# Performance work log

Measured on AMD Instinct MI355X. Metric: run time of the kernel, lower is better.

## Reference

```python
import jax, jax.numpy as jnp
import numpy as np

LN_EPS = 1e-5
N, D = 512, 512


def setup_inputs() -> dict:
    key = jax.random.key(0)
    ks = jax.random.split(key, 3)
    s1 = 1.0 / np.sqrt(2 * D)  # torch Linear default-ish scale
    s2 = 1.0 / np.sqrt(D)
    return {
        "embeddings": jax.random.normal(ks[0], (N, D), jnp.float32),
        "W1": jax.random.normal(ks[1], (2 * D, D), jnp.float32) * s1,  # [in, out]
        "b1": jnp.zeros((D,), jnp.float32),
        "gamma": jnp.ones((D,), jnp.float32),
        "beta": jnp.zeros((D,), jnp.float32),
        "W2": jax.random.normal(ks[2], (D, 1), jnp.float32) * s2,
        "b2": jnp.zeros((1,), jnp.float32),
    }


def reference(embeddings, W1, b1, gamma, beta, W2, b2):
    d = embeddings.shape[-1]
    # Linear(2D -> D) on cat(e_i, e_j) decomposes into two GEMMs + broadcast add,
    # avoiding materializing the [N, N, 2D] concatenated pair tensor.
    left = embeddings @ W1[:d]              # [N, D]  (contribution of e_i)
    right = embeddings @ W1[d:] + b1        # [N, D]  (contribution of e_j + bias)
    h = left[:, None, :] + right[None, :, :]  # [N, N, D]
    # LayerNorm over last dim (eps matches torch default)
    mu = h.mean(axis=-1, keepdims=True)
    var = ((h - mu) ** 2).mean(axis=-1, keepdims=True)
    h = (h - mu) * jax.lax.rsqrt(var + LN_EPS) * gamma + beta
    # exact GELU (torch nn.GELU default)
    h = jax.nn.gelu(h, approximate=False)
    s = jax.nn.sigmoid(jnp.squeeze(h @ W2, -1) + b2[0])  # [N, N]
    # original loop only evaluates pairs i <= j and mirrors to (j, i)
    n = s.shape[0]
    upper = jnp.arange(n)[:, None] <= jnp.arange(n)[None, :]
    return jnp.where(upper, s, s.T)
```

## Files before the change

kernel.cpp:

```cpp
#include <hip/hip_runtime.h>


#define N_ 512
#define D_ 512

__global__ __launch_bounds__(512) void k_gemm(const float* __restrict__ E,
                                              const float* __restrict__ W1,
                                              const float* __restrict__ b1,
                                              float* __restrict__ W ) {
    __shared__ float et[512 * 20];

    const int t = threadIdx.x;
    const int bg = blockIdx.x;
    const int rg = bg >> 4;
    const int cg = bg & 15;
    const int r0 = rg * 16;
    const int half = cg >> 3;
    const int cb = (cg & 7) << 6;

    for (int x = t; x < 16 * 128; x += 512) {
        const int r = x >> 7, k4 = (x & 127) << 2;
        float4 v = *(const float4*)&E[(r0 + r) * D_ + k4];
        et[(k4 + 0) * 20 + r] = v.x;
        et[(k4 + 1) * 20 + r] = v.y;
        et[(k4 + 2) * 20 + r] = v.z;
        et[(k4 + 3) * 20 + r] = v.w;
    }
    __syncthreads();

    const int lane = t & 63;
    const int ks = t >> 6;
    const int kb = ks << 6;
    const int c4 = (lane & 15) << 2;
    const int rq = ((lane >> 4) & 3) << 2;
    const float* __restrict__ wp = W1 + (half << 18) + (kb << 9) + cb + c4;

    float4 a0 = {0.f, 0.f, 0.f, 0.f}, a1 = {0.f, 0.f, 0.f, 0.f};
    float4 a2 = {0.f, 0.f, 0.f, 0.f}, a3 = {0.f, 0.f, 0.f, 0.f};
#pragma unroll 16
    for (int k = 0; k < 64; ++k) {
        float4 wv = *(const float4*)(wp + (k << 9));
        float4 ev = *(const float4*)&et[(kb + k) * 20 + rq];
        a0.x = fmaf(ev.x, wv.x, a0.x); a0.y = fmaf(ev.x, wv.y, a0.y);
        a0.z = fmaf(ev.x, wv.z, a0.z); a0.w = fmaf(ev.x, wv.w, a0.w);
        a1.x = fmaf(ev.y, wv.x, a1.x); a1.y = fmaf(ev.y, wv.y, a1.y);
        a1.z = fmaf(ev.y, wv.z, a1.z); a1.w = fmaf(ev.y, wv.w, a1.w);
        a2.x = fmaf(ev.z, wv.x, a2.x); a2.y = fmaf(ev.z, wv.y, a2.y);
        a2.z = fmaf(ev.z, wv.z, a2.z); a2.w = fmaf(ev.z, wv.w, a2.w);
        a3.x = fmaf(ev.w, wv.x, a3.x); a3.y = fmaf(ev.w, wv.y, a3.y);
        a3.z = fmaf(ev.w, wv.z, a3.z); a3.w = fmaf(ev.w, wv.w, a3.w);
    }

    __syncthreads();
    float* red = et;
    const int ob = (ks << 10) + c4;
    *(float4*)&red[ob + ((rq + 0) << 6)] = a0;
    *(float4*)&red[ob + ((rq + 1) << 6)] = a1;
    *(float4*)&red[ob + ((rq + 2) << 6)] = a2;
    *(float4*)&red[ob + ((rq + 3) << 6)] = a3;
    __syncthreads();

    float2 s = {0.f, 0.f};
#pragma unroll
    for (int k2 = 0; k2 < 8; ++k2) {
        float2 p = *(const float2*)&red[(k2 << 10) + (t << 1)];
        s.x += p.x; s.y += p.y;
    }
    const int ro = t >> 5, co = (t << 1) & 63;
    if (half) {
        float2 bb = *(const float2*)&b1[cb + co];
        s.x += bb.x; s.y += bb.y;
    }
    *(float2*)&W[((half << 9) + r0 + ro) * D_ + cb + co] = s;
}


#define GELU1(L, R, G, BE, WC, RST, T2N, ACC)                                 \
    do {                                                                      \
        float s_ = (L) + (R);                                                 \
        float x_ = fmaf(fmaf(s_, (RST), (T2N)), (G), (BE));                   \
        float q_ = x_ * fmaf(-0.10294340f, x_ * x_, -2.30220935f);            \
        float e_ = __builtin_amdgcn_exp2f(q_);                                \
        float ge_ = x_ * __builtin_amdgcn_rcpf(1.f + e_);                     \
        ACC = fmaf(ge_, (WC), ACC);                                           \
    } while (0)

#define GELU4(LQ, RQ, RST, T2N, ACC)                                          \
    do {                                                                      \
        GELU1(LQ.x, RQ.x, g4.x, be4.x, w4.x, RST, T2N, ACC);                  \
        GELU1(LQ.y, RQ.y, g4.y, be4.y, w4.y, RST, T2N, ACC);                  \
        GELU1(LQ.z, RQ.z, g4.z, be4.z, w4.z, RST, T2N, ACC);                  \
        GELU1(LQ.w, RQ.w, g4.w, be4.w, w4.w, RST, T2N, ACC);                  \
    } while (0)

#define DOT4(LQ, RQ, ACC)                                                     \
    ACC += LQ.x * RQ.x + LQ.y * RQ.y + LQ.z * RQ.z + LQ.w * RQ.w

#define BFLY(V)                                                               \
    do {                                                                      \
        V += __shfl_xor(V, 1, 64);                                            \
        V += __shfl_xor(V, 2, 64);                                            \
        V += __shfl_xor(V, 4, 64);                                            \
        V += __shfl_xor(V, 8, 64);                                            \
    } while (0)

__global__ __launch_bounds__(256, 4) void k_pair(const float* __restrict__ W,
                                                 const float* __restrict__ gf,
                                                 const float* __restrict__ bef,
                                                 const float* __restrict__ wf,
                                                 const float* __restrict__ b2f,
                                                 float* __restrict__ out) {
    __shared__ float ls[8][516];
    __shared__ float rs[8][516];
    __shared__ float smean[16];
    __shared__ float svar[16];

    const int b = blockIdx.x;
    int I = (int)((129.0f - sqrtf(16641.0f - 8.0f * (float)b)) * 0.5f);
    if (I < 0) I = 0;
    if (I > 63) I = 63;
#define S_(i) (64 * (i) - ((i) * ((i)-1)) / 2)
    while (S_(I) > b) --I;
    while (S_(I + 1) <= b) ++I;
    const int J = I + (b - S_(I));
#undef S_

    const int t = threadIdx.x;
    const int ks = t & 15;
    const int pt = t >> 4;
    const int i1 = pt & 7;
    const int j4 = (pt >> 3) * 4;
    const int Ibase = I * 8, Jbase = N_ + J * 8;

    for (int x = t; x < 8 * 128; x += 256) {
        int r = x >> 7, c4 = (x & 127) << 2;
        *(float4*)&ls[r][c4] = *(const float4*)&W[(Ibase + r) * D_ + c4];
        *(float4*)&rs[r][c4] = *(const float4*)&W[(Jbase + r) * D_ + c4];
    }
    __syncthreads();

    {
        const int lane = t & 63, w = t >> 6;
#pragma unroll
        for (int rr = 0; rr < 4; ++rr) {
            const int row = w * 4 + rr;
            const float* p = (row < 8) ? &ls[row][0] : &rs[row - 8][0];
            float4 a = *(const float4*)&p[lane << 2];
            float4 c = *(const float4*)&p[256 + (lane << 2)];
            float sm = (a.x + a.y) + (a.z + a.w) + (c.x + c.y) + (c.z + c.w);
            float sq = a.x * a.x + a.y * a.y + a.z * a.z + a.w * a.w +
                       c.x * c.x + c.y * c.y + c.z * c.z + c.w * c.w;
#pragma unroll
            for (int off = 32; off > 0; off >>= 1) {
                sm += __shfl_xor(sm, off, 64);
                sq += __shfl_xor(sq, off, 64);
            }
            if (lane == 0) {
                float mu = sm * (1.f / D_);
                smean[row] = mu;
                svar[row] = fmaf(-mu, mu, sq * (1.f / D_));
            }
        }
    }
    __syncthreads();

    float cv0 = 0.f, cv1 = 0.f, cv2 = 0.f, cv3 = 0.f;
    for (int it = 0; it < 8; ++it) {
        const int kq = (it * 16 + ks) * 4;
        float4 la = *(float4*)&ls[i1][kq];
        float4 ra = *(float4*)&rs[j4][kq];
        float4 rb = *(float4*)&rs[j4 + 1][kq];
        float4 rc = *(float4*)&rs[j4 + 2][kq];
        float4 rd = *(float4*)&rs[j4 + 3][kq];
        DOT4(la, ra, cv0); DOT4(la, rb, cv1); DOT4(la, rc, cv2); DOT4(la, rd, cv3);
    }
    BFLY(cv0); BFLY(cv1); BFLY(cv2); BFLY(cv3);

    const float ml0 = smean[i1];
    const float vl0 = svar[i1];
    const float mr0 = smean[8 + j4],     mr1 = smean[8 + j4 + 1];
    const float mr2 = smean[8 + j4 + 2], mr3 = smean[8 + j4 + 3];
    const float vr0 = svar[8 + j4],     vr1 = svar[8 + j4 + 1];
    const float vr2 = svar[8 + j4 + 2], vr3 = svar[8 + j4 + 3];
    const float rst0 = rsqrtf(vl0 + vr0 + cv0 * (2.f / D_) - 2.f * ml0 * mr0 + 1e-5f);
    const float rst1 = rsqrtf(vl0 + vr1 + cv1 * (2.f / D_) - 2.f * ml0 * mr1 + 1e-5f);
    const float rst2 = rsqrtf(vl0 + vr2 + cv2 * (2.f / D_) - 2.f * ml0 * mr2 + 1e-5f);
    const float rst3 = rsqrtf(vl0 + vr3 + cv3 * (2.f / D_) - 2.f * ml0 * mr3 + 1e-5f);
    const float t2n0 = -(ml0 + mr0) * rst0;
    const float t2n1 = -(ml0 + mr1) * rst1;
    const float t2n2 = -(ml0 + mr2) * rst2;
    const float t2n3 = -(ml0 + mr3) * rst3;

    float ac0 = 0.f, ac1 = 0.f, ac2 = 0.f, ac3 = 0.f;
    for (int it = 0; it < 8; ++it) {
        const int kq = (it * 16 + ks) * 4;
        float4 g4 = *(const float4*)&gf[kq];
        float4 be4 = *(const float4*)&bef[kq];
        float4 w4 = *(const float4*)&wf[kq];
        float4 la = *(float4*)&ls[i1][kq];
        float4 ra = *(float4*)&rs[j4][kq];
        float4 rb = *(float4*)&rs[j4 + 1][kq];
        float4 rc = *(float4*)&rs[j4 + 2][kq];
        float4 rd = *(float4*)&rs[j4 + 3][kq];
        GELU4(la, ra, rst0, t2n0, ac0); GELU4(la, rb, rst1, t2n1, ac1);
        GELU4(la, rc, rst2, t2n2, ac2); GELU4(la, rd, rst3, t2n3, ac3);
    }
    BFLY(ac0); BFLY(ac1); BFLY(ac2); BFLY(ac3);

    if (ks == 0) {
        const float bb = b2f[0];
        const float z0 = __builtin_amdgcn_rcpf(
            1.f + __builtin_amdgcn_exp2f(-1.44269504f * (ac0 + bb)));
        const float z1 = __builtin_amdgcn_rcpf(
            1.f + __builtin_amdgcn_exp2f(-1.44269504f * (ac1 + bb)));
        const float z2 = __builtin_amdgcn_rcpf(
            1.f + __builtin_amdgcn_exp2f(-1.44269504f * (ac2 + bb)));
        const float z3 = __builtin_amdgcn_rcpf(
            1.f + __builtin_amdgcn_exp2f(-1.44269504f * (ac3 + bb)));
        const int gi = Ibase + i1;
        const int gj0 = (Jbase - N_) + j4;
        if (I < J) {
            float4 o0 = {z0, z1, z2, z3};
            *(float4*)&out[gi * N_ + gj0] = o0;
            out[gj0 * N_ + gi] = z0;
            out[(gj0 + 1) * N_ + gi] = z1;
            out[(gj0 + 2) * N_ + gi] = z2;
            out[(gj0 + 3) * N_ + gi] = z3;
        } else {
            if (gi <= gj0)     { out[gi * N_ + gj0] = z0;       out[gj0 * N_ + gi] = z0; }
            if (gi <= gj0 + 1) { out[gi * N_ + gj0 + 1] = z1;   out[(gj0 + 1) * N_ + gi] = z1; }
            if (gi <= gj0 + 2) { out[gi * N_ + gj0 + 2] = z2;   out[(gj0 + 2) * N_ + gi] = z2; }
            if (gi <= gj0 + 3) { out[gi * N_ + gj0 + 3] = z3;   out[(gj0 + 3) * N_ + gi] = z3; }
        }
    }
}

extern "C" void kernel_launch(void* const* d_in, const int* in_sizes, int n_in,
                              void* d_out, int out_size, void* d_ws, size_t ws_size,
                              hipStream_t stream) {
    const float* E     = (const float*)d_in[0];
    const float* W1    = (const float*)d_in[1];
    const float* b1    = (const float*)d_in[2];
    const float* gamma = (const float*)d_in[3];
    const float* beta  = (const float*)d_in[4];
    const float* w2    = (const float*)d_in[5];
    const float* b2    = (const float*)d_in[6];
    float* out = (float*)d_out;

    float* lcrc = (float*)d_ws;

    k_gemm<<<512, 512, 0, stream>>>(E, W1, b1, lcrc);
    k_pair<<<2080, 256, 0, stream>>>(lcrc, gamma, beta, w2, b2, out);
}
```

Measured before the change: 117.4 us.

## Halve pair-kernel shared memory by staging K in two chunks

The pair kernel now stages the left and right rows in two 256-wide K chunks instead of holding all 512 columns, which halves the LDS footprint. Row statistics and cross dot products accumulate across the chunks, and the GELU pass reloads each chunk from global memory. The aim is higher occupancy and less LDS pressure per block. The cost is extra global reloads (each chunk is read twice), additional barriers, and dropping the min-blocks hint from launch bounds.

```diff
diff --git a/kernel.cpp b/kernel.cpp
--- a/kernel.cpp
+++ b/kernel.cpp
@@ -104,14 +104,44 @@
         V += __shfl_xor(V, 8, 64);                                            \
     } while (0)
 
-__global__ __launch_bounds__(256, 4) void k_pair(const float* __restrict__ W,
-                                                 const float* __restrict__ gf,
-                                                 const float* __restrict__ bef,
-                                                 const float* __restrict__ wf,
-                                                 const float* __restrict__ b2f,
-                                                 float* __restrict__ out) {
-    __shared__ float ls[8][516];
-    __shared__ float rs[8][516];
+#define RED64(V)                                                              \
+    do {                                                                      \
+        V += __shfl_xor(V, 32, 64);                                           \
+        V += __shfl_xor(V, 16, 64);                                           \
+        V += __shfl_xor(V, 8, 64);                                            \
+        V += __shfl_xor(V, 4, 64);                                            \
+        V += __shfl_xor(V, 2, 64);                                            \
+        V += __shfl_xor(V, 1, 64);                                            \
+    } while (0)
+
+#define STAGE(KB)                                                             \
+    do {                                                                      \
+        for (int x = t; x < 8 * 64; x += 256) {                               \
+            int r_ = x >> 6, c4_ = (x & 63) << 2;                             \
+            *(float4*)&ls[r_][c4_] =                                          \
+                *(const float4*)&W[(Ibase + r_) * D_ + (KB) + c4_];           \
+            *(float4*)&rs[r_][c4_] =                                          \
+                *(const float4*)&W[(Jbase + r_) * D_ + (KB) + c4_];           \
+        }                                                                     \
+    } while (0)
+
+#define STAT1(RR, SM, SQ)                                                     \
+    do {                                                                      \
+        const int row_ = (w << 2) + (RR);                                     \
+        const float* p_ = (row_ < 8) ? &ls[row_][0] : &rs[row_ - 8][0];       \
+        float4 a_ = *(const float4*)&p_[lane << 2];                           \
+        SM += (a_.x + a_.y) + (a_.z + a_.w);                                  \
+        SQ += a_.x * a_.x + a_.y * a_.y + a_.z * a_.z + a_.w * a_.w;          \
+    } while (0)
+
+__global__ __launch_bounds__(256) void k_pair(const float* __restrict__ W,
+                                              const float* __restrict__ gf,
+                                              const float* __restrict__ bef,
+                                              const float* __restrict__ wf,
+                                              const float* __restrict__ b2f,
+                                              float* __restrict__ out) {
+    __shared__ float ls[8][260];
+    __shared__ float rs[8][260];
     __shared__ float smean[16];
     __shared__ float svar[16];
 
@@ -130,51 +160,45 @@
     const int pt = t >> 4;
     const int i1 = pt & 7;
     const int j4 = (pt >> 3) * 4;
+    const int lane = t & 63, w = t >> 6;
     const int Ibase = I * 8, Jbase = N_ + J * 8;
 
-    for (int x = t; x < 8 * 128; x += 256) {
-        int r = x >> 7, c4 = (x & 127) << 2;
-        *(float4*)&ls[r][c4] = *(const float4*)&W[(Ibase + r) * D_ + c4];
-        *(float4*)&rs[r][c4] = *(const float4*)&W[(Jbase + r) * D_ + c4];
-    }
-    __syncthreads();
-
-    {
-        const int lane = t & 63, w = t >> 6;
-#pragma unroll
-        for (int rr = 0; rr < 4; ++rr) {
-            const int row = w * 4 + rr;
-            const float* p = (row < 8) ? &ls[row][0] : &rs[row - 8][0];
-            float4 a = *(const float4*)&p[lane << 2];
-            float4 c = *(const float4*)&p[256 + (lane << 2)];
-            float sm = (a.x + a.y) + (a.z + a.w) + (c.x + c.y) + (c.z + c.w);
-            float sq = a.x * a.x + a.y * a.y + a.z * a.z + a.w * a.w +
-                       c.x * c.x + c.y * c.y + c.z * c.z + c.w * c.w;
-#pragma unroll
-            for (int off = 32; off > 0; off >>= 1) {
-                sm += __shfl_xor(sm, off, 64);
-                sq += __shfl_xor(sq, off, 64);
-            }
-            if (lane == 0) {
-                float mu = sm * (1.f / D_);
-                smean[row] = mu;
-                svar[row] = fmaf(-mu, mu, sq * (1.f / D_));
-            }
+    float cv0 = 0.f, cv1 = 0.f, cv2 = 0.f, cv3 = 0.f;
+    float sm0 = 0.f, sm1 = 0.f, sm2 = 0.f, sm3 = 0.f;
+    float sq0 = 0.f, sq1 = 0.f, sq2 = 0.f, sq3 = 0.f;
+    for (int c = 0; c < 2; ++c) {
+        const int kb = c << 8;
+        STAGE(kb);
+        __syncthreads();
+        STAT1(0, sm0, sq0); STAT1(1, sm1, sq1);
+        STAT1(2, sm2, sq2); STAT1(3, sm3, sq3);
+#pragma unroll
+        for (int it = 0; it < 4; ++it) {
+            const int kq = (it * 16 + ks) * 4;
+            float4 la = *(float4*)&ls[i1][kq];
+            float4 ra = *(float4*)&rs[j4][kq];
+            float4 rb = *(float4*)&rs[j4 + 1][kq];
+            float4 rc = *(float4*)&rs[j4 + 2][kq];
+            float4 rd = *(float4*)&rs[j4 + 3][kq];
+            DOT4(la, ra, cv0); DOT4(la, rb, cv1);
+            DOT4(la, rc, cv2); DOT4(la, rd, cv3);
         }
-    }
-    __syncthreads();
-
-    float cv0 = 0.f, cv1 = 0.f, cv2 = 0.f, cv3 = 0.f;
-    for (int it = 0; it < 8; ++it) {
-        const int kq = (it * 16 + ks) * 4;
-        float4 la = *(float4*)&ls[i1][kq];
-        float4 ra = *(float4*)&rs[j4][kq];
-        float4 rb = *(float4*)&rs[j4 + 1][kq];
-        float4 rc = *(float4*)&rs[j4 + 2][kq];
-        float4 rd = *(float4*)&rs[j4 + 3][kq];
-        DOT4(la, ra, cv0); DOT4(la, rb, cv1); DOT4(la, rc, cv2); DOT4(la, rd, cv3);
-    }
+        __syncthreads();
+    }
+
+    RED64(sm0); RED64(sq0); RED64(sm1); RED64(sq1);
+    RED64(sm2); RED64(sq2); RED64(sm3); RED64(sq3);
+    if (lane == 0) {
+        float mu;
+        mu = sm0 * (1.f / D_); smean[(w << 2) + 0] = mu; svar[(w << 2) + 0] = fmaf(-mu, mu, sq0 * (1.f / D_));
+        mu = sm1 * (1.f / D_); smean[(w << 2) + 1] = mu; svar[(w << 2) + 1] = fmaf(-mu, mu, sq1 * (1.f / D_));
+        mu = sm2 * (1.f / D_); smean[(w << 2) + 2] = mu; svar[(w << 2) + 2] = fmaf(-mu, mu, sq2 * (1.f / D_));
+        mu = sm3 * (1.f / D_); smean[(w << 2) + 3] = mu; svar[(w << 2) + 3] = fmaf(-mu, mu, sq3 * (1.f / D_));
+    }
+
     BFLY(cv0); BFLY(cv1); BFLY(cv2); BFLY(cv3);
+    STAGE(0);
+    __syncthreads();
 
     const float ml0 = smean[i1];
     const float vl0 = svar[i1];
@@ -192,11 +216,29 @@
     const float t2n3 = -(ml0 + mr3) * rst3;
 
     float ac0 = 0.f, ac1 = 0.f, ac2 = 0.f, ac3 = 0.f;
-    for (int it = 0; it < 8; ++it) {
+#pragma unroll
+    for (int it = 0; it < 4; ++it) {
         const int kq = (it * 16 + ks) * 4;
         float4 g4 = *(const float4*)&gf[kq];
         float4 be4 = *(const float4*)&bef[kq];
         float4 w4 = *(const float4*)&wf[kq];
+        float4 la = *(float4*)&ls[i1][kq];
+        float4 ra = *(float4*)&rs[j4][kq];
+        float4 rb = *(float4*)&rs[j4 + 1][kq];
+        float4 rc = *(float4*)&rs[j4 + 2][kq];
+        float4 rd = *(float4*)&rs[j4 + 3][kq];
+        GELU4(la, ra, rst0, t2n0, ac0); GELU4(la, rb, rst1, t2n1, ac1);
+        GELU4(la, rc, rst2, t2n2, ac2); GELU4(la, rd, rst3, t2n3, ac3);
+    }
+    __syncthreads();
+    STAGE(256);
+    __syncthreads();
+#pragma unroll
+    for (int it = 0; it < 4; ++it) {
+        const int kq = (it * 16 + ks) * 4;
+        float4 g4 = *(const float4*)&gf[256 + kq];
+        float4 be4 = *(const float4*)&bef[256 + kq];
+        float4 w4 = *(const float4*)&wf[256 + kq];
         float4 la = *(float4*)&ls[i1][kq];
         float4 ra = *(float4*)&rs[j4][kq];
         float4 rb = *(float4*)&rs[j4 + 1][kq];
```

Result: slower. 120.1 us (+2.3%).
